# Optimization experiments

Hardware: AMD Instinct MI355X
Metric: run time of the kernel (lower is better)

The kernel has to match this reference:

```python
import jax, jax.numpy as jnp
import numpy as np

UP = 8  # nn.Upsample(scale_factor=8), nearest


def _affine_grid(theta, H, W):
    # torch F.affine_grid, align_corners=False: pixel-center normalized coords
    xs = (jnp.arange(W, dtype=jnp.float32) + 0.5) * (2.0 / W) - 1.0
    ys = (jnp.arange(H, dtype=jnp.float32) + 0.5) * (2.0 / H) - 1.0
    base = jnp.stack([
        jnp.broadcast_to(xs[None, :], (H, W)),
        jnp.broadcast_to(ys[:, None], (H, W)),
        jnp.ones((H, W), jnp.float32),
    ], axis=-1)  # [H,W,3] = (x, y, 1)
    return jnp.einsum('hwk,bjk->bhwj', base, theta)  # [B,H,W,2], last dim = (x, y)


def _grid_sample(img, grid):
    # bilinear, padding_mode='zeros', align_corners=False (torch defaults)
    B, C, H, W = img.shape
    ix = ((grid[..., 0] + 1.0) * W - 1.0) * 0.5  # [B,Ho,Wo]
    iy = ((grid[..., 1] + 1.0) * H - 1.0) * 0.5
    ix0 = jnp.floor(ix)
    iy0 = jnp.floor(iy)
    wx1 = ix - ix0
    wy1 = iy - iy0

    def corner(xc, yc, w):
        valid = (xc >= 0) & (xc <= W - 1) & (yc >= 0) & (yc <= H - 1)
        xk = jnp.clip(xc, 0, W - 1).astype(jnp.int32)
        yk = jnp.clip(yc, 0, H - 1).astype(jnp.int32)
        g = jax.vmap(lambda im, yy, xx: im[:, yy, xx])(img, yk, xk)  # [B,C,Ho,Wo]
        return g * (w * valid.astype(img.dtype))[:, None, :, :]

    return (corner(ix0, iy0, (1.0 - wx1) * (1.0 - wy1))
            + corner(ix0 + 1.0, iy0, wx1 * (1.0 - wy1))
            + corner(ix0, iy0 + 1.0, (1.0 - wx1) * wy1)
            + corner(ix0 + 1.0, iy0 + 1.0, wx1 * wy1))


def setup_inputs() -> dict:
    key = jax.random.key(0)
    k1, k2 = jax.random.split(key)
    gt = jax.random.normal(k1, (8, 1, 128, 256), dtype=jnp.float32)
    theta = jax.random.normal(k2, (8, 6), dtype=jnp.float32)
    return {"gt": gt, "theta": theta, "output_sizex": 2048, "output_sizey": 1024}


def reference(gt, theta, output_sizex, output_sizey):
    onlyy = jnp.array([0., 0., 0., 0., 1., 1.], jnp.float32)
    offset = jnp.array([1., 0., 0., 0., 0., 0.], jnp.float32)
    thetay = (theta * onlyy + offset).reshape(-1, 2, 3)  # [[1,0,0],[0,t4,t5]]
    th = theta.reshape(-1, 2, 3)
    # nearest upsample x8
    gt_up = jnp.repeat(jnp.repeat(gt, UP, axis=2), UP, axis=3)
    grid = _affine_grid(th, output_sizey, output_sizex)
    box = _grid_sample(gt_up, grid)
    gridy = _affine_grid(thetay, output_sizey, output_sizex)
    boxy = _grid_sample(gt_up, gridy)
    return (box, boxy)
```

## Files before the change

### kernel.cpp

```cpp
#include <hip/hip_runtime.h>
#include <stdint.h>


typedef float vfloat4 __attribute__((ext_vector_type(4)));

constexpr int BATCH = 8;
constexpr int HI = 128, WI = 256;
constexpr int HO = 1024, WO = 2048;
constexpr size_t NPIX = (size_t)BATCH * HO * WO;
constexpr int PH = HI + 2;
constexpr int PSTRIDE = 264;
constexpr size_t PIMG = (size_t)PH * PSTRIDE;

__global__ __launch_bounds__(256) void pad_kernel(
    const float* __restrict__ gt, float* __restrict__ P)
{
    const int i = blockIdx.x * 256 + threadIdx.x;
    if (i >= (int)(BATCH * PIMG)) return;
    const int b  = i / (int)PIMG;
    const int r  = i - b * (int)PIMG;
    const int y  = r / PSTRIDE - 1;
    const int x  = r - (r / PSTRIDE) * PSTRIDE - 1;
    float v = 0.0f;
    if (y >= 0 && y < HI && x >= 0 && x < WI)
        v = gt[(size_t)b * HI * WI + y * WI + x];
    P[i] = v;
}

__global__ __launch_bounds__(256) void stn_kernel(
    const float* __restrict__ gt,
    const float* __restrict__ theta,
    const float* __restrict__ P,
    float* __restrict__ out)
{
    const int row = blockIdx.x;
    const int b = row >> 10;
    const int h = row & (HO - 1);
    const int t = threadIdx.x;
    const int w0 = t << 3;

    const float* tb = theta + b * 6;
    const float t0 = tb[0], t1 = tb[1], t2 = tb[2];
    const float t3 = tb[3], t4 = tb[4], t5 = tb[5];
    const float* __restrict__ gtb = gt + b * (HI * WI);
    const float* __restrict__ Pb  = P + (size_t)b * PIMG + PSTRIDE + 1;

    const float ys = (h + 0.5f) * (2.0f / (float)HO) - 1.0f;

    {
        const float gy2 = t4 * ys + t5;
        const float iy = ((gy2 + 1.0f) * (float)HO - 1.0f) * 0.5f;
        const float fy = floorf(iy);
        const float wy = iy - fy;
        const float vy0 = (fy >= 0.0f && fy <= (float)(HO - 1)) ? 1.0f : 0.0f;
        const float vy1 = (fy >= -1.0f && fy <= (float)(HO - 2)) ? 1.0f : 0.0f;
        const int y0 = ((int)fminf(fmaxf(fy,        0.0f), (float)(HO - 1))) >> 3;
        const int y1 = ((int)fminf(fmaxf(fy + 1.0f, 0.0f), (float)(HO - 1))) >> 3;
        const float s0 = gtb[y0 * WI + t];
        const float s1 = gtb[y1 * WI + t];
        const float byv = s0 * ((1.0f - wy) * vy0) + s1 * (wy * vy1);
        const vfloat4 vb = {byv, byv, byv, byv};
        vfloat4* dst = reinterpret_cast<vfloat4*>(out + NPIX + (size_t)row * WO + w0);
        __builtin_nontemporal_store(vb, dst);
        __builtin_nontemporal_store(vb, dst + 1);
    }

    const float xn0 = (w0 + 0.5f) * (2.0f / (float)WO) - 1.0f;
    const float gx0 = t0 * xn0 + (t1 * ys + t2);
    const float gy0 = t3 * xn0 + (t4 * ys + t5);
    float ix = ((gx0 + 1.0f) * (float)WO - 1.0f) * 0.5f;
    float iy = ((gy0 + 1.0f) * (float)HO - 1.0f) * 0.5f;
    const float dix = t0;
    const float diy = 0.5f * t3;

    float px[8];
#pragma unroll
    for (int p = 0; p < 8; ++p) {
        const float fx = floorf(ix), fy = floorf(iy);
        const float wx = ix - fx,    wy = iy - fy;
        const int xi = (int)fx, yi = (int)fy;
        const int cx0 = min(max(xi >> 3,       -1), WI);
        const int cx1 = min(max((xi + 1) >> 3, -1), WI);
        const int cy0 = min(max(yi >> 3,       -1), HI);
        const int cy1 = min(max((yi + 1) >> 3, -1), HI);
        const float* __restrict__ r0 = Pb + cy0 * PSTRIDE;
        const float* __restrict__ r1 = Pb + cy1 * PSTRIDE;
        const float a = r0[cx0], bb = r0[cx1];
        const float c = r1[cx0], d  = r1[cx1];
        const float h0 = fmaf(wx, bb - a, a);
        const float h1 = fmaf(wx, d - c,  c);
        px[p] = fmaf(wy, h1 - h0, h0);
        ix += dix; iy += diy;
    }
    vfloat4* dst = reinterpret_cast<vfloat4*>(out + (size_t)row * WO + w0);
    const vfloat4 v0 = {px[0], px[1], px[2], px[3]};
    const vfloat4 v1 = {px[4], px[5], px[6], px[7]};
    __builtin_nontemporal_store(v0, dst);
    __builtin_nontemporal_store(v1, dst + 1);
}

extern "C" void kernel_launch(void* const* d_in, const int* in_sizes, int n_in,
                              void* d_out, int out_size, void* d_ws, size_t ws_size,
                              hipStream_t stream) {
    const float* gt    = (const float*)d_in[0];
    const float* theta = (const float*)d_in[1];
    float* out = (float*)d_out;
    float* P   = (float*)d_ws;

    const int padN = (int)(BATCH * PIMG);
    pad_kernel<<<(padN + 255) / 256, 256, 0, stream>>>(gt, P);
    stn_kernel<<<BATCH * HO, 256, 0, stream>>>(gt, theta, P, out);
}
```

Before: 173.6 us.

## Pack 2x2 neighborhoods into float4 table and skip fully out-of-range segments

The padding pass now writes a float4 per source cell holding its 2x2 neighborhood, so each bilinear sample needs one 16-byte gather instead of four scalar loads. Duplicate-corner cases are handled with selects. A per-thread early-out writes zeros when all eight samples fall outside the image. In exchange the workspace is four times larger and the pad pass does more work.

```diff
diff --git a/kernel.cpp b/kernel.cpp
--- a/kernel.cpp
+++ b/kernel.cpp
@@ -8,29 +8,33 @@
 constexpr int HI = 128, WI = 256;
 constexpr int HO = 1024, WO = 2048;
 constexpr size_t NPIX = (size_t)BATCH * HO * WO;
-constexpr int PH = HI + 2;
-constexpr int PSTRIDE = 264;
-constexpr size_t PIMG = (size_t)PH * PSTRIDE;
 
-__global__ __launch_bounds__(256) void pad_kernel(
-    const float* __restrict__ gt, float* __restrict__ P)
+constexpr int QH = HI + 2;
+constexpr int QW = WI + 2;
+constexpr size_t QIMG = (size_t)QH * QW;
+
+__global__ __launch_bounds__(256) void pad4_kernel(
+    const float* __restrict__ gt, vfloat4* __restrict__ Q)
 {
     const int i = blockIdx.x * 256 + threadIdx.x;
-    if (i >= (int)(BATCH * PIMG)) return;
-    const int b  = i / (int)PIMG;
-    const int r  = i - b * (int)PIMG;
-    const int y  = r / PSTRIDE - 1;
-    const int x  = r - (r / PSTRIDE) * PSTRIDE - 1;
-    float v = 0.0f;
-    if (y >= 0 && y < HI && x >= 0 && x < WI)
-        v = gt[(size_t)b * HI * WI + y * WI + x];
-    P[i] = v;
+    if (i >= (int)(BATCH * QIMG)) return;
+    const int b = i / (int)QIMG;
+    const int r = i - b * (int)QIMG;
+    const int y = r / QW - 1;
+    const int x = r - (r / QW) * QW - 1;
+    const float* __restrict__ g = gt + (size_t)b * (HI * WI);
+    auto val = [&](int yy, int xx) -> float {
+        return (yy >= 0 && yy < HI && xx >= 0 && xx < WI)
+                   ? g[yy * WI + xx] : 0.0f;
+    };
+    vfloat4 q = { val(y, x), val(y, x + 1), val(y + 1, x), val(y + 1, x + 1) };
+    Q[i] = q;
 }
 
 __global__ __launch_bounds__(256) void stn_kernel(
     const float* __restrict__ gt,
     const float* __restrict__ theta,
-    const float* __restrict__ P,
+    const vfloat4* __restrict__ Q,
     float* __restrict__ out)
 {
     const int row = blockIdx.x;
@@ -43,7 +47,7 @@
     const float t0 = tb[0], t1 = tb[1], t2 = tb[2];
     const float t3 = tb[3], t4 = tb[4], t5 = tb[5];
     const float* __restrict__ gtb = gt + b * (HI * WI);
-    const float* __restrict__ Pb  = P + (size_t)b * PIMG + PSTRIDE + 1;
+    const vfloat4* __restrict__ Qb = Q + (size_t)b * QIMG;
 
     const float ys = (h + 0.5f) * (2.0f / (float)HO) - 1.0f;
 
@@ -73,24 +77,39 @@
     const float dix = t0;
     const float diy = 0.5f * t3;
 
+    const float ixe = ix + 7.0f * dix;
+    const float iye = iy + 7.0f * diy;
+    const bool segzero =
+        (fmaxf(ix, ixe) < -1.0f) || (fminf(ix, ixe) >= (float)WO) ||
+        (fmaxf(iy, iye) < -1.0f) || (fminf(iy, iye) >= (float)HO);
+
     float px[8];
+    if (segzero) {
 #pragma unroll
-    for (int p = 0; p < 8; ++p) {
-        const float fx = floorf(ix), fy = floorf(iy);
-        const float wx = ix - fx,    wy = iy - fy;
-        const int xi = (int)fx, yi = (int)fy;
-        const int cx0 = min(max(xi >> 3,       -1), WI);
-        const int cx1 = min(max((xi + 1) >> 3, -1), WI);
-        const int cy0 = min(max(yi >> 3,       -1), HI);
-        const int cy1 = min(max((yi + 1) >> 3, -1), HI);
-        const float* __restrict__ r0 = Pb + cy0 * PSTRIDE;
-        const float* __restrict__ r1 = Pb + cy1 * PSTRIDE;
-        const float a = r0[cx0], bb = r0[cx1];
-        const float c = r1[cx0], d  = r1[cx1];
-        const float h0 = fmaf(wx, bb - a, a);
-        const float h1 = fmaf(wx, d - c,  c);
-        px[p] = fmaf(wy, h1 - h0, h0);
-        ix += dix; iy += diy;
+        for (int p = 0; p < 8; ++p) px[p] = 0.0f;
+    } else {
+#pragma unroll
+        for (int p = 0; p < 8; ++p) {
+            const float fx = floorf(ix), fy = floorf(iy);
+            const float wx = ix - fx,    wy = iy - fy;
+            const int xi = (int)fx, yi = (int)fy;
+            const int cx0 = min(max(xi >> 3,       -1), WI);
+            const int cx1 = min(max((xi + 1) >> 3, -1), WI);
+            const int cy0 = min(max(yi >> 3,       -1), HI);
+            const int cy1 = min(max((yi + 1) >> 3, -1), HI);
+            const vfloat4 q = Qb[(cy0 + 1) * QW + (cx0 + 1)];
+            const bool cxe = (cx1 == cx0);
+            const bool cye = (cy1 == cy0);
+            const float a  = q.x;
+            const float bb = cxe ? q.x : q.y;
+            const float c  = cye ? q.x : q.z;
+            const float dl = cxe ? q.z : q.w;
+            const float d  = cye ? bb  : dl;
+            const float h0 = fmaf(wx, bb - a, a);
+            const float h1 = fmaf(wx, d - c,  c);
+            px[p] = fmaf(wy, h1 - h0, h0);
+            ix += dix; iy += diy;
+        }
     }
     vfloat4* dst = reinterpret_cast<vfloat4*>(out + (size_t)row * WO + w0);
     const vfloat4 v0 = {px[0], px[1], px[2], px[3]};
@@ -105,9 +124,9 @@
     const float* gt    = (const float*)d_in[0];
     const float* theta = (const float*)d_in[1];
     float* out = (float*)d_out;
-    float* P   = (float*)d_ws;
+    vfloat4* Q = (vfloat4*)d_ws;
 
-    const int padN = (int)(BATCH * PIMG);
-    pad_kernel<<<(padN + 255) / 256, 256, 0, stream>>>(gt, P);
-    stn_kernel<<<BATCH * HO, 256, 0, stream>>>(gt, theta, P, out);
+    const int qN = (int)(BATCH * QIMG);
+    pad4_kernel<<<(qN + 255) / 256, 256, 0, stream>>>(gt, Q);
+    stn_kernel<<<BATCH * HO, 256, 0, stream>>>(gt, theta, Q, out);
 }
```

Measured after the change: 168.4 us. 1.03x faster.
